# Kernel tuning notes

Hardware: AMD Instinct MI355X
Metric: run time of the kernel (lower is better)

## Reference

```python
import jax, jax.numpy as jnp
from jax import lax
import numpy as np

HIDDEN = 768
NUM_LABELS = 17
B, T = 64, 512


def setup_inputs() -> dict:
    key = jax.random.key(0)
    k1, k2, k3, k4, k5, k6, k7, k8 = jax.random.split(key, 8)
    outputs = jax.random.normal(k1, (B, T, HIDDEN), dtype=jnp.float32)
    labels = jax.random.randint(k2, (B, T), 0, NUM_LABELS, dtype=jnp.int64)
    # left-contiguous mask from random lengths in [T//4, T]; mask[:,0] always True
    lengths = jax.random.randint(k3, (B,), T // 4, T + 1)
    mask = (jnp.arange(T)[None, :] < lengths[:, None])
    # parameters (nn.Linear + torchcrf CRF params)
    bound = 1.0 / np.sqrt(HIDDEN)
    fc_w = jax.random.uniform(k4, (NUM_LABELS, HIDDEN), jnp.float32, -bound, bound)
    fc_b = jax.random.uniform(k5, (NUM_LABELS,), jnp.float32, -bound, bound)
    start_trans = jax.random.uniform(k6, (NUM_LABELS,), jnp.float32, -0.1, 0.1)
    end_trans = jax.random.uniform(k7, (NUM_LABELS,), jnp.float32, -0.1, 0.1)
    trans = jax.random.uniform(k8, (NUM_LABELS, NUM_LABELS), jnp.float32, -0.1, 0.1)
    return {"outputs": outputs, "fc_w": fc_w, "fc_b": fc_b,
            "start_trans": start_trans, "end_trans": end_trans, "trans": trans,
            "labels": labels, "mask": mask}


def _crf_llh(emissions, tags, mask, start_trans, end_trans, trans):
    # emissions: [B,T,K], tags: [B,T] int, mask: [B,T] bool (left-contiguous, col 0 True)
    Bn, Tn, K = emissions.shape
    maskf = mask.astype(emissions.dtype)
    # ----- numerator: score of the gold path -----
    em_tag = jnp.take_along_axis(emissions, tags[:, :, None], axis=2)[:, :, 0]  # [B,T]
    num = start_trans[tags[:, 0]] + em_tag[:, 0]
    trans_steps = trans[tags[:, :-1], tags[:, 1:]]                               # [B,T-1]
    num = num + jnp.sum((trans_steps + em_tag[:, 1:]) * maskf[:, 1:], axis=1)
    seq_ends = mask.sum(axis=1).astype(jnp.int32) - 1
    last_tags = tags[jnp.arange(Bn), seq_ends]
    num = num + end_trans[last_tags]
    # ----- denominator: forward algorithm (log partition) -----
    def step(score, xs):
        em_i, m_i = xs  # [B,K], [B]
        # broadcast: score over source tag, trans [K,K], emission over target tag
        nxt = jax.nn.logsumexp(score[:, :, None] + trans[None, :, :] + em_i[:, None, :], axis=1)
        score = jnp.where(m_i[:, None], nxt, score)
        return score, None
    init = start_trans[None, :] + emissions[:, 0]                                # [B,K]
    score, _ = lax.scan(step,
                        init,
                        (jnp.swapaxes(emissions[:, 1:], 0, 1),                   # [T-1,B,K]
                         jnp.swapaxes(mask[:, 1:], 0, 1)))                        # [T-1,B]
    denom = jax.nn.logsumexp(score + end_trans[None, :], axis=1)                 # [B]
    return num - denom


def reference(outputs, fc_w, fc_b, start_trans, end_trans, trans, labels, mask):
    emissions = jnp.einsum('bth,kh->btk', outputs, fc_w) + fc_b                  # [B,T,K]
    mask = mask.at[:, 0].set(True)
    tags = jnp.where(labels == -100, 0, labels)
    llh = _crf_llh(emissions, tags, mask, start_trans, end_trans, trans)
    loss = -jnp.mean(llh)   # torchcrf reduction='mean' = mean over batch
    return emissions, loss
```

## Files before the change

### kernel.cpp

```cpp
#include <hip/hip_runtime.h>

#define HID 768
#define NL  17
#define BB  64
#define TT  512

#define SEG  16
#define SLEN 32
#define QST  352

typedef __attribute__((ext_vector_type(8))) short bf16x8;
typedef __attribute__((ext_vector_type(4))) float f32x4;

__device__ __forceinline__ unsigned cvtpk(float a, float b) {
    unsigned r;
    asm("v_cvt_pk_bf16_f32 %0, %1, %2" : "=v"(r) : "v"(a), "v"(b));
    return r;
}

__global__ __launch_bounds__(256) void emis_kernel(const float* __restrict__ x,
                                                   const float* __restrict__ w,
                                                   const float* __restrict__ bias,
                                                   float* __restrict__ y) {
    __shared__ unsigned short WP[2][18][776];

    const int tid = threadIdx.x;

    for (int e = tid; e < 776; e += 256) { WP[0][17][e] = 0; WP[1][17][e] = 0; }
#pragma unroll
    for (int j = 0; j < 13; ++j) {
        const int g4 = tid + 256 * j;
        if (g4 < 3264) {
            const float4 f = *reinterpret_cast<const float4*>(w + 4 * g4);
            const int col = g4 / 192;
            const int e   = (g4 - col * 192) * 4;
            const unsigned h0 = cvtpk(f.x, f.y);
            const unsigned h1 = cvtpk(f.z, f.w);
            const unsigned l0 = cvtpk(f.x - __uint_as_float(h0 << 16),
                                      f.y - __uint_as_float(h0 & 0xFFFF0000u));
            const unsigned l1 = cvtpk(f.z - __uint_as_float(h1 << 16),
                                      f.w - __uint_as_float(h1 & 0xFFFF0000u));
            uint2 hv; hv.x = h0; hv.y = h1;
            uint2 lv; lv.x = l0; lv.y = l1;
            *reinterpret_cast<uint2*>(&WP[0][col][e]) = hv;
            *reinterpret_cast<uint2*>(&WP[1][col][e]) = lv;
        }
    }
    __syncthreads();

    const int lane = tid & 63;
    const int c0   = lane & 15;
    int c1 = 16 + c0; if (c1 > 17) c1 = 17;
    const int kg   = (lane >> 4) * 8;
    const int mtile = blockIdx.x * 4 + (tid >> 6);
    const float* xp = x + (size_t)(mtile * 16 + c0) * HID + kg;

    const int roff = (blockIdx.x + 6 * (tid >> 6)) % 24;

    const unsigned short* pH0 = &WP[0][c0][kg];
    const unsigned short* pH1 = &WP[0][c1][kg];
    const unsigned short* pL0 = &WP[1][c0][kg];
    const unsigned short* pL1 = &WP[1][c1][kg];

    f32x4 acc0 = {0.f, 0.f, 0.f, 0.f};
    f32x4 acc1 = {0.f, 0.f, 0.f, 0.f};

#define TE(T)   ((T) + roff < 24 ? (T) + roff : (T) + roff - 24)
#define LDX(T)  (*reinterpret_cast<const float4*>(xp + 32 * TE(T)))
#define LDX4(T) (*reinterpret_cast<const float4*>(xp + 32 * TE(T) + 4))

#define XSTEP(Q0, Q1, T)                                                      \
    {                                                                         \
        const int LK = 32 * TE(T);                      \
        union { unsigned u[4]; bf16x8 v; } H_, L_;                            \
        H_.u[0] = cvtpk(Q0.x, Q0.y);                                          \
        H_.u[1] = cvtpk(Q0.z, Q0.w);                                          \
        H_.u[2] = cvtpk(Q1.x, Q1.y);                                          \
        H_.u[3] = cvtpk(Q1.z, Q1.w);                                          \
        L_.u[0] = cvtpk(Q0.x - __uint_as_float(H_.u[0] << 16),                \
                        Q0.y - __uint_as_float(H_.u[0] & 0xFFFF0000u));       \
        L_.u[1] = cvtpk(Q0.z - __uint_as_float(H_.u[1] << 16),                \
                        Q0.w - __uint_as_float(H_.u[1] & 0xFFFF0000u));       \
        L_.u[2] = cvtpk(Q1.x - __uint_as_float(H_.u[2] << 16),                \
                        Q1.y - __uint_as_float(H_.u[2] & 0xFFFF0000u));       \
        L_.u[3] = cvtpk(Q1.z - __uint_as_float(H_.u[3] << 16),                \
                        Q1.w - __uint_as_float(H_.u[3] & 0xFFFF0000u));       \
        const bf16x8 bh0 = *reinterpret_cast<const bf16x8*>(pH0 + LK);        \
        const bf16x8 bh1 = *reinterpret_cast<const bf16x8*>(pH1 + LK);        \
        const bf16x8 bl0 = *reinterpret_cast<const bf16x8*>(pL0 + LK);        \
        const bf16x8 bl1 = *reinterpret_cast<const bf16x8*>(pL1 + LK);        \
        acc0 = __builtin_amdgcn_mfma_f32_16x16x32_bf16(H_.v, bh0, acc0, 0, 0, 0); \
        acc0 = __builtin_amdgcn_mfma_f32_16x16x32_bf16(H_.v, bl0, acc0, 0, 0, 0); \
        acc0 = __builtin_amdgcn_mfma_f32_16x16x32_bf16(L_.v, bh0, acc0, 0, 0, 0); \
        acc1 = __builtin_amdgcn_mfma_f32_16x16x32_bf16(H_.v, bh1, acc1, 0, 0, 0); \
        acc1 = __builtin_amdgcn_mfma_f32_16x16x32_bf16(H_.v, bl1, acc1, 0, 0, 0); \
        acc1 = __builtin_amdgcn_mfma_f32_16x16x32_bf16(L_.v, bh1, acc1, 0, 0, 0); \
    }

    float4 qA0 = LDX(0), qA1 = LDX4(0);
    float4 qB0 = LDX(1), qB1 = LDX4(1);
    float4 qC0 = LDX(2), qC1 = LDX4(2);
    float4 qD0 = LDX(3), qD1 = LDX4(3);

#pragma unroll
    for (int t = 0; t < 24; t += 4) {
        XSTEP(qA0, qA1, t)
        if (t + 4 < 24) { qA0 = LDX(t + 4); qA1 = LDX4(t + 4); }
        XSTEP(qB0, qB1, t + 1)
        if (t + 5 < 24) { qB0 = LDX(t + 5); qB1 = LDX4(t + 5); }
        XSTEP(qC0, qC1, t + 2)
        if (t + 6 < 24) { qC0 = LDX(t + 6); qC1 = LDX4(t + 6); }
        XSTEP(qD0, qD1, t + 3)
        if (t + 7 < 24) { qD0 = LDX(t + 7); qD1 = LDX4(t + 7); }
    }
#undef XSTEP
#undef LDX
#undef LDX4
#undef TE

    const float bc  = bias[c0];
    const float b16 = bias[16];
    const int   rb  = mtile * 16 + (lane >> 4) * 4;
#pragma unroll
    for (int i = 0; i < 4; ++i) {
        const int row = rb + i;
        y[(size_t)row * NL + c0] = acc0[i] + bc;
        if (c0 == 0) y[(size_t)row * NL + 16] = acc1[i] + b16;
    }
}

__global__ __launch_bounds__(64) void crf_scan_kernel(const float* __restrict__ emis,
                                                      const float* __restrict__ tr_,
                                                      const int* __restrict__ mask,
                                                      float* __restrict__ ws) {
    __shared__ float QT[2][18][20];

    const int bs = blockIdx.x;
    const int b  = bs >> 4;
    const int s  = bs & 15;
    const int l  = threadIdx.x;
    const float* eb = emis + (size_t)b * TT * NL;

    int lenp = 0;
#pragma unroll
    for (int m = 0; m < 8; ++m) lenp += (mask[b * TT + l + 64 * m] != 0);
#pragma unroll
    for (int off = 32; off; off >>= 1) lenp += __shfl_down(lenp, off);
    const int len = __shfl(lenp, 0);

    const int t0    = 1 + SLEN * s;
    const int tend  = min(t0 + SLEN, len);
    const int trips = (tend > t0) ? (tend - t0) : 0;

    const bool act = (l < 51);
    const int  i   = act ? (l / 3) : 0;
    const int  m   = act ? (l - 3 * (l / 3)) : 0;
    const int  j0  = 6 * m;

    if (act) {
#pragma unroll
        for (int jj = 0; jj < 6; ++jj)
            QT[0][j0 + jj][i] = (i == j0 + jj) ? 1.f : 0.f;
    }

    float at[17];
#pragma unroll
    for (int k = 0; k < 17; ++k) at[k] = __expf(tr_[k * NL + i]);

    float psc = 1.f;
    int   Mi  = 0;
    float emv = (trips > 0) ? eb[t0 * NL + i] : 0.f;
    int   t   = t0;

#define QSTEP(SRC, DST, TCUR)                                                 \
    {                                                                         \
        const float e_ = __expf(emv) * psc;  psc = 1.f;                       \
        const int tn_ = ((TCUR) + 1 < tend) ? ((TCUR) + 1) : (TT - 1);        \
        const float env_ = eb[tn_ * NL + i];                                  \
        float o[6];                                                           \
        _Pragma("unroll")                                                     \
        for (int jj = 0; jj < 6; ++jj) {                                      \
            const float* qr = &QT[SRC][j0 + jj][0];                           \
            const float4 a0 = *reinterpret_cast<const float4*>(qr);           \
            const float4 a1 = *reinterpret_cast<const float4*>(qr + 4);       \
            const float4 a2 = *reinterpret_cast<const float4*>(qr + 8);       \
            const float4 a3 = *reinterpret_cast<const float4*>(qr + 12);      \
            const float aL  = qr[16];                                         \
            float u0 = at[0] * a0.x, u1 = at[1] * a0.y;                       \
            float u2 = at[2] * a0.z, u3 = at[3] * a0.w;                       \
            u0 = fmaf(at[4],  a1.x, u0); u1 = fmaf(at[5],  a1.y, u1);         \
            u2 = fmaf(at[6],  a1.z, u2); u3 = fmaf(at[7],  a1.w, u3);         \
            u0 = fmaf(at[8],  a2.x, u0); u1 = fmaf(at[9],  a2.y, u1);         \
            u2 = fmaf(at[10], a2.z, u2); u3 = fmaf(at[11], a2.w, u3);         \
            u0 = fmaf(at[12], a3.x, u0); u1 = fmaf(at[13], a3.y, u1);         \
            u2 = fmaf(at[14], a3.z, u2); u3 = fmaf(at[15], a3.w, u3);         \
            u0 = fmaf(at[16], aL,   u0);                                      \
            o[jj] = (u0 + u1) + (u2 + u3);                                    \
        }                                                                     \
        if (act) {                                                            \
            _Pragma("unroll")                                                 \
            for (int jj = 0; jj < 6; ++jj)                                    \
                QT[DST][j0 + jj][i] = e_ * o[jj];                             \
        }                                                                     \
        emv = env_;                                                           \
    }

    for (int pp = 0; pp < (trips >> 1); ++pp) {
        QSTEP(0, 1, t)
        QSTEP(1, 0, t + 1)
        t += 2;
        const float q00 = QT[0][0][0];
        const int E = (int)((__float_as_uint(q00) >> 23) & 0xff) - 127;
        Mi += E;
        psc = __builtin_amdgcn_ldexpf(1.f, -E);
    }
    int sbuf = 0;
    if (trips & 1) { QSTEP(0, 1, t) sbuf = 1; }
#undef QSTEP

    if (act) {
        float* dst = ws + (size_t)bs * QST + i * 20;
#pragma unroll
        for (int jj = 0; jj < 6; ++jj) {
            const int j = j0 + jj;
            if (j < 17) dst[j] = psc * QT[sbuf][j][i];
        }
    }
    if (l == 0) ws[(size_t)bs * QST + 340] = (float)Mi;
}

__device__ __forceinline__ float bcast(float v, int i) {
    return __uint_as_float(__builtin_amdgcn_readlane(__float_as_uint(v), i));
}

__global__ __launch_bounds__(64) void crf_combine_kernel(const float* __restrict__ emis,
                                                         const float* __restrict__ st_,
                                                         const float* __restrict__ en_,
                                                         const float* __restrict__ tr_,
                                                         const int* __restrict__ labels,
                                                         const int* __restrict__ mask,
                                                         const float* __restrict__ ws,
                                                         float* __restrict__ llh) {
    const int b = blockIdx.x;
    const int l = threadIdx.x;
    const float* eb = emis + (size_t)b * TT * NL;
    const int*   lb = labels + b * TT;

    int lenp = 0;
#pragma unroll
    for (int m = 0; m < 8; ++m) lenp += (mask[b * TT + l + 64 * m] != 0);
#pragma unroll
    for (int off = 32; off; off >>= 1) lenp += __shfl_down(lenp, off);
    const int len = __shfl(lenp, 0);

    float np = 0.f;
#pragma unroll
    for (int m = 0; m < 8; ++m) {
        const int t = l + 64 * m;
        int tag = lb[t]; if ((unsigned)tag >= NL) tag = 0;
        if (t < len) {
            if (t == 0) {
                np += st_[tag] + eb[tag];
            } else {
                int tp = lb[t - 1]; if ((unsigned)tp >= NL) tp = 0;
                np += tr_[tp * NL + tag] + eb[t * NL + tag];
            }
            if (t == len - 1) np += en_[tag];
        }
    }
#pragma unroll
    for (int off = 32; off; off >>= 1) np += __shfl_down(np, off);
    const float num = __shfl(np, 0);

    const bool act = (l < NL);
    const int  j   = act ? l : 0;

    float p  = act ? __expf(st_[j] + eb[j]) : 0.f;
    int   Mi = 0;

    for (int s = 0; s < SEG; ++s) {
        const float* qs = ws + (size_t)(b * SEG + s) * QST;
        const float* qr = qs + j * 20;
        const float4 a0 = *reinterpret_cast<const float4*>(qr);
        const float4 a1 = *reinterpret_cast<const float4*>(qr + 4);
        const float4 a2 = *reinterpret_cast<const float4*>(qr + 8);
        const float4 a3 = *reinterpret_cast<const float4*>(qr + 12);
        const float  aL = qr[16];
        const float  Msc = qs[340];

        float u0 = a0.x * bcast(p, 0),  u1 = a0.y * bcast(p, 1);
        float u2 = a0.z * bcast(p, 2),  u3 = a0.w * bcast(p, 3);
        u0 = fmaf(a1.x, bcast(p, 4),  u0); u1 = fmaf(a1.y, bcast(p, 5),  u1);
        u2 = fmaf(a1.z, bcast(p, 6),  u2); u3 = fmaf(a1.w, bcast(p, 7),  u3);
        u0 = fmaf(a2.x, bcast(p, 8),  u0); u1 = fmaf(a2.y, bcast(p, 9),  u1);
        u2 = fmaf(a2.z, bcast(p, 10), u2); u3 = fmaf(a2.w, bcast(p, 11), u3);
        u0 = fmaf(a3.x, bcast(p, 12), u0); u1 = fmaf(a3.y, bcast(p, 13), u1);
        u2 = fmaf(a3.z, bcast(p, 14), u2); u3 = fmaf(a3.w, bcast(p, 15), u3);
        u0 = fmaf(aL,   bcast(p, 16), u0);
        p = act ? ((u0 + u1) + (u2 + u3)) : 0.f;
        Mi += (int)Msc;

        const unsigned pb = (unsigned)__builtin_amdgcn_readlane((int)__float_as_uint(p), 0);
        const int e = (int)((pb >> 23) & 0xff) - 127;
        Mi += e;
        p = __builtin_amdgcn_ldexpf(p, -e);
    }

    float v = act ? p * __expf(en_[j]) : 0.f;
#pragma unroll
    for (int off = 32; off; off >>= 1) v += __shfl_down(v, off);

    if (l == 0) {
        const float denom = (float)Mi * 0.6931471805599453f + __logf(v);
        llh[b] = num - denom;
    }
}

__global__ __launch_bounds__(64) void loss_kernel(const float* __restrict__ llh,
                                                  float* __restrict__ loss) {
    float v = llh[threadIdx.x];
#pragma unroll
    for (int off = 32; off; off >>= 1) v += __shfl_down(v, off);
    if (threadIdx.x == 0) loss[0] = -(v * (1.0f / BB));
}

extern "C" void kernel_launch(void* const* d_in, const int* in_sizes, int n_in,
                              void* d_out, int out_size, void* d_ws, size_t ws_size,
                              hipStream_t stream) {
    const float* outputs = (const float*)d_in[0];
    const float* fc_w    = (const float*)d_in[1];
    const float* fc_b    = (const float*)d_in[2];
    const float* start_t = (const float*)d_in[3];
    const float* end_t   = (const float*)d_in[4];
    const float* trans   = (const float*)d_in[5];
    const int*   labels  = (const int*)d_in[6];
    const int*   mask    = (const int*)d_in[7];

    float* emis = (float*)d_out;
    float* loss = emis + (size_t)BB * TT * NL;
    float* ws   = (float*)d_ws;
    float* llh  = ws + (size_t)BB * SEG * QST;

    emis_kernel<<<(BB * TT) / 64, 256, 0, stream>>>(outputs, fc_w, fc_b, emis);
    crf_scan_kernel<<<BB * SEG, 64, 0, stream>>>(emis, trans, mask, ws);
    crf_combine_kernel<<<BB, 64, 0, stream>>>(emis, start_t, end_t, trans,
                                              labels, mask, ws, llh);
    loss_kernel<<<1, 64, 0, stream>>>(llh, loss);
}
```

Before: 55.91 us.

## Fuse CRF segment scan into emission GEMM kernel via shared-memory emissions

```diff
diff --git a/kernel.cpp b/kernel.cpp
--- a/kernel.cpp
+++ b/kernel.cpp
@@ -18,11 +18,16 @@
     return r;
 }
 
-__global__ __launch_bounds__(256) void emis_kernel(const float* __restrict__ x,
-                                                   const float* __restrict__ w,
-                                                   const float* __restrict__ bias,
-                                                   float* __restrict__ y) {
+__global__ __launch_bounds__(256) void emis_scan_kernel(const float* __restrict__ x,
+                                                        const float* __restrict__ w,
+                                                        const float* __restrict__ bias,
+                                                        const int* __restrict__ mask,
+                                                        const float* __restrict__ tr_,
+                                                        float* __restrict__ y,
+                                                        float* __restrict__ ws) {
     __shared__ unsigned short WP[2][18][776];
+    __shared__ float em_s[64][20];
+    __shared__ float QT[2][2][18][20];
 
     const int tid = threadIdx.x;
 
@@ -52,10 +57,9 @@
     const int c0   = lane & 15;
     int c1 = 16 + c0; if (c1 > 17) c1 = 17;
     const int kg   = (lane >> 4) * 8;
-    const int mtile = blockIdx.x * 4 + (tid >> 6);
+    const int mloc = tid >> 6;
+    const int mtile = blockIdx.x * 4 + mloc;
     const float* xp = x + (size_t)(mtile * 16 + c0) * HID + kg;
-
-    const int roff = (blockIdx.x + 6 * (tid >> 6)) % 24;
 
     const unsigned short* pH0 = &WP[0][c0][kg];
     const unsigned short* pH1 = &WP[0][c1][kg];
@@ -65,13 +69,12 @@
     f32x4 acc0 = {0.f, 0.f, 0.f, 0.f};
     f32x4 acc1 = {0.f, 0.f, 0.f, 0.f};
 
-#define TE(T)   ((T) + roff < 24 ? (T) + roff : (T) + roff - 24)
-#define LDX(T)  (*reinterpret_cast<const float4*>(xp + 32 * TE(T)))
-#define LDX4(T) (*reinterpret_cast<const float4*>(xp + 32 * TE(T) + 4))
+#define LDX(T)  (*reinterpret_cast<const float4*>(xp + 32 * (T)))
+#define LDX4(T) (*reinterpret_cast<const float4*>(xp + 32 * (T) + 4))
 
 #define XSTEP(Q0, Q1, T)                                                      \
     {                                                                         \
-        const int LK = 32 * TE(T);                      \
+        const int LK = 32 * (T);                                              \
         union { unsigned u[4]; bf16x8 v; } H_, L_;                            \
         H_.u[0] = cvtpk(Q0.x, Q0.y);                                          \
         H_.u[1] = cvtpk(Q0.z, Q0.w);                                          \
@@ -116,71 +119,74 @@
 #undef XSTEP
 #undef LDX
 #undef LDX4
-#undef TE
 
     const float bc  = bias[c0];
     const float b16 = bias[16];
     const int   rb  = mtile * 16 + (lane >> 4) * 4;
+    const int   lr  = mloc * 16 + (lane >> 4) * 4;
 #pragma unroll
     for (int i = 0; i < 4; ++i) {
         const int row = rb + i;
-        y[(size_t)row * NL + c0] = acc0[i] + bc;
-        if (c0 == 0) y[(size_t)row * NL + 16] = acc1[i] + b16;
-    }
-}
-
-__global__ __launch_bounds__(64) void crf_scan_kernel(const float* __restrict__ emis,
-                                                      const float* __restrict__ tr_,
-                                                      const int* __restrict__ mask,
-                                                      float* __restrict__ ws) {
-    __shared__ float QT[2][18][20];
-
-    const int bs = blockIdx.x;
-    const int b  = bs >> 4;
-    const int s  = bs & 15;
-    const int l  = threadIdx.x;
-    const float* eb = emis + (size_t)b * TT * NL;
-
-    int lenp = 0;
-#pragma unroll
-    for (int m = 0; m < 8; ++m) lenp += (mask[b * TT + l + 64 * m] != 0);
-#pragma unroll
-    for (int off = 32; off; off >>= 1) lenp += __shfl_down(lenp, off);
-    const int len = __shfl(lenp, 0);
-
-    const int t0    = 1 + SLEN * s;
-    const int tend  = min(t0 + SLEN, len);
-    const int trips = (tend > t0) ? (tend - t0) : 0;
-
-    const bool act = (l < 51);
-    const int  i   = act ? (l / 3) : 0;
-    const int  m   = act ? (l - 3 * (l / 3)) : 0;
-    const int  j0  = 6 * m;
-
-    if (act) {
-#pragma unroll
-        for (int jj = 0; jj < 6; ++jj)
-            QT[0][j0 + jj][i] = (i == j0 + jj) ? 1.f : 0.f;
-    }
-
-    float at[17];
-#pragma unroll
-    for (int k = 0; k < 17; ++k) at[k] = __expf(tr_[k * NL + i]);
-
-    float psc = 1.f;
-    int   Mi  = 0;
-    float emv = (trips > 0) ? eb[t0 * NL + i] : 0.f;
-    int   t   = t0;
-
-#define QSTEP(SRC, DST, TCUR)                                                 \
+        const float v0 = acc0[i] + bc;
+        y[(size_t)row * NL + c0] = v0;
+        em_s[lr + i][c0] = v0;
+        if (c0 == 0) {
+            const float v1 = acc1[i] + b16;
+            y[(size_t)row * NL + 16] = v1;
+            em_s[lr + i][16] = v1;
+        }
+    }
+    __syncthreads();
+
+    const int widx = tid >> 6;
+    if (widx >= 2) return;
+    {
+        const int l  = lane;
+        const int b  = blockIdx.x >> 3;
+        const int q8 = blockIdx.x & 7;
+        const int sl = (q8 << 1) + widx;
+        const int T0 = q8 << 6;
+
+        int lenp = 0;
+#pragma unroll
+        for (int m = 0; m < 8; ++m) lenp += (mask[b * TT + l + 64 * m] != 0);
+#pragma unroll
+        for (int off = 32; off; off >>= 1) lenp += __shfl_down(lenp, off);
+        const int len = __shfl(lenp, 0);
+
+        const int tstart = (32 * sl > 1) ? 32 * sl : 1;
+        int tend = 32 * sl + 32; if (tend > len) tend = len;
+        const int trips = tend - tstart;
+
+        const bool act = (l < 51);
+        const int  i   = act ? (l / 3) : 0;
+        const int  m3  = act ? (l - 3 * (l / 3)) : 0;
+        const int  j0  = 6 * m3;
+
+        if (act) {
+#pragma unroll
+            for (int jj = 0; jj < 6; ++jj)
+                QT[widx][0][j0 + jj][i] = (i == j0 + jj) ? 1.f : 0.f;
+        }
+
+        float at[17];
+#pragma unroll
+        for (int k = 0; k < 17; ++k) at[k] = __expf(tr_[k * NL + i]);
+
+        float psc = 1.f;
+        int   Mi  = 0;
+        float emv = (trips > 0) ? em_s[tstart - T0][i] : 0.f;
+        int   t   = tstart;
+
+#define QSTEPF(SRC, DST, TCUR)                                                \
     {                                                                         \
         const float e_ = __expf(emv) * psc;  psc = 1.f;                       \
-        const int tn_ = ((TCUR) + 1 < tend) ? ((TCUR) + 1) : (TT - 1);        \
-        const float env_ = eb[tn_ * NL + i];                                  \
+        int ln_ = (TCUR) + 1 - T0; ln_ = (ln_ < 63) ? ln_ : 63;               \
+        const float env_ = em_s[ln_][i];                                      \
         float o[6];                                                           \
         _Pragma("unroll")                                                     \
         for (int jj = 0; jj < 6; ++jj) {                                      \
-            const float* qr = &QT[SRC][j0 + jj][0];                           \
+            const float* qr = &QT[widx][SRC][j0 + jj][0];                     \
             const float4 a0 = *reinterpret_cast<const float4*>(qr);           \
             const float4 a1 = *reinterpret_cast<const float4*>(qr + 4);       \
             const float4 a2 = *reinterpret_cast<const float4*>(qr + 8);       \
@@ -200,33 +206,35 @@
         if (act) {                                                            \
             _Pragma("unroll")                                                 \
             for (int jj = 0; jj < 6; ++jj)                                    \
-                QT[DST][j0 + jj][i] = e_ * o[jj];                             \
+                QT[widx][DST][j0 + jj][i] = e_ * o[jj];                       \
         }                                                                     \
         emv = env_;                                                           \
     }
 
-    for (int pp = 0; pp < (trips >> 1); ++pp) {
-        QSTEP(0, 1, t)
-        QSTEP(1, 0, t + 1)
-        t += 2;
-        const float q00 = QT[0][0][0];
-        const int E = (int)((__float_as_uint(q00) >> 23) & 0xff) - 127;
-        Mi += E;
-        psc = __builtin_amdgcn_ldexpf(1.f, -E);
-    }
-    int sbuf = 0;
-    if (trips & 1) { QSTEP(0, 1, t) sbuf = 1; }
-#undef QSTEP
-
-    if (act) {
-        float* dst = ws + (size_t)bs * QST + i * 20;
-#pragma unroll
-        for (int jj = 0; jj < 6; ++jj) {
-            const int j = j0 + jj;
-            if (j < 17) dst[j] = psc * QT[sbuf][j][i];
-        }
-    }
-    if (l == 0) ws[(size_t)bs * QST + 340] = (float)Mi;
+        for (int pp = 0; pp < (trips >> 1); ++pp) {
+            QSTEPF(0, 1, t)
+            QSTEPF(1, 0, t + 1)
+            t += 2;
+            const float q00 = QT[widx][0][0][0];
+            const int E = (int)((__float_as_uint(q00) >> 23) & 0xff) - 127;
+            Mi += E;
+            psc = __builtin_amdgcn_ldexpf(1.f, -E);
+        }
+        int sbuf = 0;
+        if (trips > 0 && (trips & 1)) { QSTEPF(0, 1, t) sbuf = 1; }
+#undef QSTEPF
+
+        const int bs = b * SEG + sl;
+        if (act) {
+            float* dst = ws + (size_t)bs * QST + i * 20;
+#pragma unroll
+            for (int jj = 0; jj < 6; ++jj) {
+                const int j = j0 + jj;
+                if (j < 17) dst[j] = psc * QT[widx][sbuf][j][i];
+            }
+        }
+        if (l == 0) ws[(size_t)bs * QST + 340] = (float)Mi;
+    }
 }
 
 __device__ __forceinline__ float bcast(float v, int i) {
@@ -341,8 +349,8 @@
     float* ws   = (float*)d_ws;
     float* llh  = ws + (size_t)BB * SEG * QST;
 
-    emis_kernel<<<(BB * TT) / 64, 256, 0, stream>>>(outputs, fc_w, fc_b, emis);
-    crf_scan_kernel<<<BB * SEG, 64, 0, stream>>>(emis, trans, mask, ws);
+    emis_scan_kernel<<<(BB * TT) / 64, 256, 0, stream>>>(outputs, fc_w, fc_b,
+                                                         mask, trans, emis, ws);
     crf_combine_kernel<<<BB, 64, 0, stream>>>(emis, start_t, end_t, trans,
                                               labels, mask, ws, llh);
     loss_kernel<<<1, 64, 0, stream>>>(llh, loss);
```

After: 53.97 us. -3.5%, faster.
